# Kernel optimization log

Hardware: AMD Instinct MI355X
Metric: run time of the kernel (lower is better)

The kernel has to match this reference:

```python
import jax, jax.numpy as jnp
import numpy as np

CUTOFFS = [0, 19997, 39997, 199997, 267735]  # cutoff_ends
SIZES = [19997, 20000, 160000, 67738]
DEMBS = [1024, 256, 64, 16]  # d_embed // div_val**i, div_val=4
N, D_PROJ = 1024, 1024


def setup_inputs() -> dict:
    key = jax.random.key(0)
    ks = jax.random.split(key, 20)
    inp = {
        "hidden": jax.random.normal(ks[0], (N, D_PROJ), jnp.float32),
        "target": jax.random.randint(ks[1], (N,), 0, CUTOFFS[-1], dtype=jnp.int64),
    }
    for i in range(4):
        inp[f"W{i}"] = 0.02 * jax.random.normal(ks[2 + 3 * i], (SIZES[i], DEMBS[i]), jnp.float32)
        inp[f"b{i}"] = jnp.zeros((SIZES[i],), jnp.float32)
        inp[f"p{i}"] = 0.02 * jax.random.normal(ks[3 + 3 * i], (D_PROJ, DEMBS[i]), jnp.float32)
    inp["cluster_weight"] = 0.02 * jax.random.normal(ks[14], (3, DEMBS[0]), jnp.float32)
    inp["cluster_bias"] = jnp.zeros((3,), jnp.float32)
    return inp


def _logit(hidden, W, b, p):
    # einsum('bd,de,ev->bv', hidden, proj, weight.T) + bias
    return (hidden @ p) @ W.T + b


def reference(hidden, target, W0, b0, p0, W1, b1, p1, W2, b2, p2, W3, b3, p3,
              cluster_weight, cluster_bias):
    n = hidden.shape[0]
    rows = jnp.arange(n)
    shortlist = W0.shape[0]  # 19997

    # head cluster: shortlist vocab + 3 cluster logits
    head_w = jnp.concatenate([W0, cluster_weight], axis=0)   # [shortlist+3, d_embed]
    head_b = jnp.concatenate([b0, cluster_bias], axis=0)
    head_lp = jax.nn.log_softmax(_logit(hidden, head_w, head_b, p0), axis=-1)  # [N, shortlist+3]

    masks = [target < CUTOFFS[1]]
    lps = [head_lp[rows, jnp.clip(target, 0, shortlist - 1)]]

    for i, (W, b, p) in enumerate([(W1, b1, p1), (W2, b2, p2), (W3, b3, p3)], start=1):
        l_idx, r_idx = CUTOFFS[i], CUTOFFS[i + 1]
        tail_lp = jax.nn.log_softmax(_logit(hidden, W, b, p), axis=-1)  # [N, r-l]
        rel = jnp.clip(target - l_idx, 0, r_idx - l_idx - 1)
        lps.append(head_lp[:, shortlist + i - 1] + tail_lp[rows, rel])
        masks.append((target >= l_idx) & (target < r_idx))

    logprob = jnp.select(masks, lps)
    return -logprob  # nll, shape [N]
```

## Files before the change

### kernel.cpp

```cpp
#include <hip/hip_runtime.h>
#include <stdint.h>

typedef short v8s __attribute__((ext_vector_type(8)));
typedef float f4 __attribute__((ext_vector_type(4)));
typedef unsigned short u16;
typedef unsigned int u32;

#define CUT1 19997
#define CUT2 39997
#define CUT3 199997
#define NROWS 1024
#define LDP 1360

#define NG_HEAD 157
#define NG_T1 40
#define NG_T2 157
#define NG_T3 67

__device__ __forceinline__ u32 pack2(float a, float b) {
    return (__float_as_uint(a) >> 16) | (__float_as_uint(b) & 0xffff0000u);
}
__device__ __forceinline__ float b2f(u16 h) { return __uint_as_float(((u32)h) << 16); }
__device__ __forceinline__ u16 f2b(float f) { return (u16)(__float_as_uint(f) >> 16); }

__device__ __forceinline__ void gload16(const void* g, void* l) {
    __builtin_amdgcn_global_load_lds(
        (const __attribute__((address_space(1))) u32*)g,
        (__attribute__((address_space(3))) u32*)l, 16, 0, 0);
}

__device__ __forceinline__ void cast8(const float* __restrict__ in, u16* __restrict__ out, size_t j) {
    const float4* p = (const float4*)(in + j * 8);
    float4 a = p[0], b = p[1];
    uint4 o = { pack2(a.x, a.y), pack2(a.z, a.w), pack2(b.x, b.y), pack2(b.z, b.w) };
    *(uint4*)(out + j * 8) = o;
}

__global__ __launch_bounds__(256) void prep_small_k(
    const float* __restrict__ hidden,
    const float* __restrict__ p0, const float* __restrict__ p1,
    const float* __restrict__ p2, const float* __restrict__ p3,
    const int* __restrict__ target,
    u16* __restrict__ hb, u16* __restrict__ pTb,
    int* __restrict__ cnt, int* __restrict__ slot,
    int* __restrict__ rowmap)
{
    int bid = blockIdx.x;
    int tid = threadIdx.x;

    if (bid < 512) {
        cast8(hidden, hb, bid * 256 + tid);
        return;
    }
    if (bid < 1888) {
        int b = bid - 512;
        const float* src; int d, rowOff, bx, by;
        if (b < 1024)      { src = p0; d = 1024; rowOff = 0;    bx = b & 31;          by = b >> 5; }
        else if (b < 1280) { src = p1; d = 256;  rowOff = 1024; bx = (b - 1024) & 7;  by = (b - 1024) >> 3; }
        else if (b < 1344) { src = p2; d = 64;   rowOff = 1280; bx = (b - 1280) & 1;  by = (b - 1280) >> 1; }
        else               { src = p3; d = 16;   rowOff = 1344; bx = 0;               by = b - 1344; }
        __shared__ float tile[32][33];
        int tx = tid & 31, ty = tid >> 5;
        int x = bx * 32 + tx;
        int ybase = by * 32;
#pragma unroll
        for (int j = 0; j < 4; ++j) {
            int r = ty + j * 8;
            tile[r][tx] = (x < d) ? src[(size_t)(ybase + r) * d + x] : 0.f;
        }
        __syncthreads();
#pragma unroll
        for (int j = 0; j < 4; ++j) {
            int x2 = bx * 32 + ty + j * 8;
            if (x2 < d) pTb[(size_t)(rowOff + x2) * 1024 + ybase + tx] = f2b(tile[tx][ty + j * 8]);
        }
        return;
    }

    __shared__ int lcnt[3];
    for (int i = tid; i < 3072; i += 256) rowmap[i] = 0;
    if (tid < 3) lcnt[tid] = 0;
    __syncthreads();
    for (int r = tid; r < NROWS; r += 256) {
        int t = target[r];
        int c = (t < CUT1) ? -1 : (t < CUT2) ? 0 : (t < CUT3) ? 1 : 2;
        int s = -1;
        if (c >= 0) {
            s = atomicAdd(&lcnt[c], 1);
            rowmap[c * 1024 + s] = r;
        }
        slot[r] = s;
    }
    __syncthreads();
    if (tid < 3) cnt[tid] = lcnt[tid];
}

template<int MODE, int NCOL, int K>
__device__ __forceinline__ void gemm_body(
    u16* __restrict__ As, u16* __restrict__ Bs, float* __restrict__ bsm,
    const u16* __restrict__ A, int lda, const int* __restrict__ rowmap,
    const u16* __restrict__ B, int ldb,
    const float* __restrict__ bias, int N,
    u16* __restrict__ Cout, int ldc,
    float* __restrict__ pout, const int* __restrict__ count,
    int bx, int byg)
{
    constexpr int nk = K / 32;
    constexpr int total = NCOL * nk;

    const int tid = threadIdx.x;
    const int rbase = bx * 128;
    if (MODE == 1 && count) {
        int c = *count;
        if (rbase >= ((c + 127) & ~127)) return;
    }
    const int wave = tid >> 6, lane = tid & 63;
    const int l4 = lane & 15, quad = lane >> 4;
    const int wg = (wave >> 1) * 4;
    const int cg = (wave & 1) * 4;
    const int wr = wg * 16, wc = cg * 16;

    const int g0 = tid >> 6, seg0 = (tid >> 4) & 3, r0 = tid & 15;
    const int s1i = 256 + tid;
    const int g1 = s1i >> 6, seg1 = (s1i >> 4) & 3, r1 = s1i & 15;

    const u16 *Asrc0, *Asrc1;
    {
        int ar0 = rbase + g0 * 16 + r0, ar1 = rbase + g1 * 16 + r1;
        if (rowmap) { ar0 = rowmap[ar0]; ar1 = rowmap[ar1]; }
        Asrc0 = A + (size_t)ar0 * lda + seg0 * 8;
        Asrc1 = A + (size_t)ar1 * lda + seg1 * 8;
    }

    if (MODE == 1) {
        const int cb0 = byg * (NCOL * 128);
        for (int i2 = tid; i2 < NCOL * 128; i2 += 256) {
            int col = cb0 + i2;
            bsm[i2] = (col < N) ? bias[col] : 0.f;
        }
        __syncthreads();
    }

    auto stage = [&](int s2) {
        const int buf = s2 % 3;
        const int kk = (s2 % nk) * 32;
        const int ct = s2 / nk;
        const int cb = (byg * NCOL + ct) * 128;
        int bc0 = cb + g0 * 16 + r0; if (bc0 >= N) bc0 = N - 1;
        int bc1 = cb + g1 * 16 + r1; if (bc1 >= N) bc1 = N - 1;
        u16* bA = As + buf * 4096;
        u16* bB = Bs + buf * 4096;
        gload16(Asrc0 + kk, bA + tid * 8);
        gload16(Asrc1 + kk, bA + (256 + tid) * 8);
        gload16(B + (size_t)bc0 * ldb + seg0 * 8 + kk, bB + tid * 8);
        gload16(B + (size_t)bc1 * ldb + seg1 * 8 + kk, bB + (256 + tid) * 8);
    };

    float part[4][4];
    if (MODE == 1) {
#pragma unroll
        for (int r = 0; r < 4; ++r)
#pragma unroll
            for (int g = 0; g < 4; ++g) part[r][g] = 0.f;
    }

    stage(0);
    if (total > 1) stage(1);

    const f4 zero4 = {0.f, 0.f, 0.f, 0.f};
    f4 acc[4][4];

#pragma unroll
    for (int s = 0; s < total; ++s) {
        if (s + 1 < total) asm volatile("s_waitcnt vmcnt(4)" ::: "memory");
        else               asm volatile("s_waitcnt vmcnt(0)" ::: "memory");
        __builtin_amdgcn_sched_barrier(0);
        __builtin_amdgcn_s_barrier();
        __builtin_amdgcn_sched_barrier(0);

        const int buf = s % 3;
        const u16* Ab = As + buf * 4096;
        const u16* Bb = Bs + buf * 4096;
        v8s af[4], bf[4];
#pragma unroll
        for (int r = 0; r < 4; ++r)
            af[r] = *(const v8s*)&Ab[((wg + r) * 64 + quad * 16 + l4) * 8];
#pragma unroll
        for (int c = 0; c < 4; ++c)
            bf[c] = *(const v8s*)&Bb[((cg + c) * 64 + quad * 16 + l4) * 8];

        if (s + 2 < total) stage(s + 2);

        if ((s % nk) == 0) {
#pragma unroll
            for (int r = 0; r < 4; ++r)
#pragma unroll
                for (int c = 0; c < 4; ++c) acc[r][c] = zero4;
        }

        __builtin_amdgcn_s_setprio(1);
#pragma unroll
        for (int r = 0; r < 4; ++r)
#pragma unroll
            for (int c = 0; c < 4; ++c)
                acc[r][c] = __builtin_amdgcn_mfma_f32_16x16x32_bf16(af[r], bf[c], acc[r][c], 0, 0, 0);
        __builtin_amdgcn_s_setprio(0);

        if ((s % nk) == nk - 1) {
            const int ct = s / nk;
            const int cbase = (byg * NCOL + ct) * 128;
            if (MODE == 0) {
#pragma unroll
                for (int c = 0; c < 4; ++c) {
                    int col = cbase + wc + c * 16 + l4;
                    if (col < N) {
#pragma unroll
                        for (int r = 0; r < 4; ++r)
#pragma unroll
                            for (int g = 0; g < 4; ++g) {
                                int row = rbase + wr + r * 16 + quad * 4 + g;
                                Cout[(size_t)row * ldc + col] = f2b(acc[r][c][g]);
                            }
                    }
                }
            } else {
#pragma unroll
                for (int c = 0; c < 4; ++c) {
                    int col = cbase + wc + c * 16 + l4;
                    if (col < N) {
                        float bb = bsm[ct * 128 + wc + c * 16 + l4];
#pragma unroll
                        for (int r = 0; r < 4; ++r)
#pragma unroll
                            for (int g = 0; g < 4; ++g)
                                part[r][g] += __expf(acc[r][c][g] + bb);
                    }
                }
            }
        }
    }

    if (MODE == 1) {
#pragma unroll
        for (int off = 1; off < 16; off <<= 1)
#pragma unroll
            for (int r = 0; r < 4; ++r)
#pragma unroll
                for (int g = 0; g < 4; ++g)
                    part[r][g] += __shfl_xor(part[r][g], off);
        float v = part[0][0];
#pragma unroll
        for (int r = 0; r < 4; ++r)
#pragma unroll
            for (int g = 0; g < 4; ++g)
                if (l4 == r * 4 + g) v = part[r][g];
        int rowoff = (l4 >> 2) * 16 + quad * 4 + (l4 & 3);
        float* lbuf = (float*)As;
        __syncthreads();
        lbuf[(wave & 1) * 128 + wr + rowoff] = v;
        __syncthreads();
        if (tid < 128) pout[rbase + tid] = lbuf[tid] + lbuf[128 + tid];
    }
}

#define CP_E0 2559616
#define CP_E1 3199616
#define CP_E2 4479616
__global__ __launch_bounds__(256, 3) void castproj_k(
    const u16* __restrict__ hb, const u16* __restrict__ pTb, u16* __restrict__ proj,
    const float* __restrict__ W0, const float* __restrict__ W1,
    const float* __restrict__ W2, const float* __restrict__ W3,
    u16* __restrict__ W0b, u16* __restrict__ W1b,
    u16* __restrict__ W2b, u16* __restrict__ W3b)
{
    __shared__ __align__(16) u16 As[3 * 4096];
    __shared__ __align__(16) u16 Bs[3 * 4096];
    int bid = blockIdx.x;
    if (bid < 128) {
        int x = bid & 7, j = bid >> 3;
        int byg = x * 2 + (j >> 3), bx = j & 7;
        if (byg >= 11) return;
        gemm_body<0, 1, 1024>(As, Bs, nullptr, hb, 1024, nullptr, pTb, 1024, nullptr, 1360,
                              proj, LDP, nullptr, nullptr, bx, byg);
        return;
    }
    int i = (bid - 128) * 256 + threadIdx.x;
    if (i < CP_E0) { cast8(W0, W0b, i); return; }
    if (i < CP_E1) { cast8(W1, W1b, i - CP_E0); return; }
    if (i < CP_E2) { cast8(W2, W2b, i - CP_E1); return; }
    int r = i - CP_E2;
    if (r >= 67738) return;
    const float4* p = (const float4*)(W3 + (size_t)r * 16);
    float4 a = p[0], b = p[1], c = p[2], d = p[3];
    uint4 o0 = { pack2(a.x, a.y), pack2(a.z, a.w), pack2(b.x, b.y), pack2(b.z, b.w) };
    uint4 o1 = { pack2(c.x, c.y), pack2(c.z, c.w), pack2(d.x, d.y), pack2(d.z, d.w) };
    uint4 z = { 0, 0, 0, 0 };
    uint4* q = (uint4*)(W3b + (size_t)r * 32);
    q[0] = o0; q[1] = o1; q[2] = z; q[3] = z;
}

#define SE_GRID 3456
__global__ __launch_bounds__(256, 3) void sumexp_k(
    const u16* __restrict__ proj,
    const u16* __restrict__ W0b, const u16* __restrict__ W1b,
    const u16* __restrict__ W2b, const u16* __restrict__ W3b,
    const float* __restrict__ b0, const float* __restrict__ b1,
    const float* __restrict__ b2, const float* __restrict__ b3,
    float* __restrict__ Ph, float* __restrict__ Pt1,
    float* __restrict__ Pt2, float* __restrict__ Pt3,
    const int* __restrict__ rmap, const int* __restrict__ cnt)
{
    __shared__ __align__(16) u16 As[3 * 4096];
    __shared__ __align__(16) u16 Bs[3 * 4096];
    __shared__ __align__(16) float bsm[1024];
    int bid = blockIdx.x;
    if (bid < 1280) {
        int x = bid & 7, j = bid >> 3;
        int byg = x * 20 + (j >> 3), bx = j & 7;
        if (byg >= NG_HEAD) return;
        gemm_body<1, 1, 1024>(As, Bs, bsm, proj, LDP, nullptr, W0b, 1024, b0, CUT1,
                              nullptr, 0, Ph + (size_t)byg * 1024, nullptr, bx, byg);
    } else if (bid < 1600) {
        int rel = bid - 1280;
        int x = rel & 7, j = rel >> 3;
        int byg = x * 5 + (j >> 3), bx = j & 7;
        gemm_body<1, 4, 256>(As, Bs, bsm, proj + 1024, LDP, rmap, W1b, 256, b1, 20000,
                             nullptr, 0, Pt1 + (size_t)byg * 1024, cnt + 0, bx, byg);
    } else if (bid < 2880) {
        int rel = bid - 1600;
        int x = rel & 7, j = rel >> 3;
        int byg = x * 20 + (j >> 3), bx = j & 7;
        if (byg >= NG_T2) return;
        gemm_body<1, 8, 64>(As, Bs, bsm, proj + 1280, LDP, rmap + 1024, W2b, 64, b2, 160000,
                            nullptr, 0, Pt2 + (size_t)byg * 1024, cnt + 1, bx, byg);
    } else {
        int rel = bid - 2880;
        int x = rel & 7, j = rel >> 3;
        int byg = x * 9 + (j >> 3), bx = j & 7;
        if (byg >= NG_T3) return;
        gemm_body<1, 8, 32>(As, Bs, bsm, proj + 1344, LDP, rmap + 2048, W3b, 32, b3, 67738,
                            nullptr, 0, Pt3 + (size_t)byg * 1024, cnt + 2, bx, byg);
    }
}

__global__ __launch_bounds__(256) void final_k(
    const u16* __restrict__ proj, const int* __restrict__ target, const int* __restrict__ slot,
    const float* __restrict__ cw, const float* __restrict__ cb,
    const float* __restrict__ W0, const float* __restrict__ b0,
    const float* __restrict__ W1, const float* __restrict__ b1,
    const float* __restrict__ W2, const float* __restrict__ b2,
    const float* __restrict__ W3, const float* __restrict__ b3,
    const float* __restrict__ Ph, const float* __restrict__ Pt1,
    const float* __restrict__ Pt2, const float* __restrict__ Pt3,
    float* __restrict__ out)
{
    int row = blockIdx.x * 4 + (threadIdx.x >> 6);
    int lane = threadIdx.x & 63;
    const u16* pr = proj + (size_t)row * LDP;

    float c0 = 0.f, c1 = 0.f, c2 = 0.f;
    for (int k = lane; k < 1024; k += 64) {
        float pv = b2f(pr[k]);
        c0 += pv * cw[k]; c1 += pv * cw[1024 + k]; c2 += pv * cw[2048 + k];
    }
    float hs = 0.f;
    for (int g = lane; g < NG_HEAD; g += 64) hs += Ph[g * 1024 + row];

    int t = target[row];
    const float* W; const float* bb; int K, off, rel;
    const float* Pc = Ph; int gc = 0;
    if (t < CUT1)      { W = W0; bb = b0; K = 1024; off = 0;    rel = t; }
    else if (t < CUT2) { W = W1; bb = b1; K = 256;  off = 1024; rel = t - CUT1; Pc = Pt1; gc = NG_T1; }
    else if (t < CUT3) { W = W2; bb = b2; K = 64;   off = 1280; rel = t - CUT2; Pc = Pt2; gc = NG_T2; }
    else               { W = W3; bb = b3; K = 16;   off = 1344; rel = t - CUT3; Pc = Pt3; gc = NG_T3; }

    float ts = 0.f;
    int s = slot[row];
    if (s >= 0) {
        for (int g = lane; g < gc; g += 64) ts += Pc[g * 1024 + s];
    }
    float acc = 0.f;
    const float* wr = W + (size_t)rel * K;
    for (int k = lane; k < K; k += 64) acc += b2f(pr[off + k]) * wr[k];

#pragma unroll
    for (int o2 = 1; o2 < 64; o2 <<= 1) {
        c0 += __shfl_xor(c0, o2); c1 += __shfl_xor(c1, o2); c2 += __shfl_xor(c2, o2);
        hs += __shfl_xor(hs, o2); ts += __shfl_xor(ts, o2); acc += __shfl_xor(acc, o2);
    }

    if (lane == 0) {
        c0 += cb[0]; c1 += cb[1]; c2 += cb[2];
        float tl = acc + bb[rel];
        float lseh = __logf(hs + __expf(c0) + __expf(c1) + __expf(c2));
        float lp;
        if (t < CUT1) lp = tl - lseh;
        else {
            int c = (t < CUT2) ? 0 : (t < CUT3) ? 1 : 2;
            float cc = (c == 0) ? c0 : (c == 1) ? c1 : c2;
            lp = (cc - lseh) + (tl - __logf(ts));
        }
        out[row] = -lp;
    }
}

__global__ void cast_bf16_k(const float* __restrict__ in, u16* __restrict__ out, int n8) {
    int i = blockIdx.x * 256 + threadIdx.x;
    if (i >= n8) return;
    cast8(in, out, i);
}

__global__ void transpose_f_k(const float* __restrict__ in, float* __restrict__ out, int d, int rowOff) {
    __shared__ float tile[32][33];
    int tx = threadIdx.x, ty = threadIdx.y;
    int x = blockIdx.x * 32 + tx;
    int ybase = blockIdx.y * 32;
#pragma unroll
    for (int j = 0; j < 4; ++j) {
        int r = ty + j * 8;
        tile[r][tx] = (x < d) ? in[(size_t)(ybase + r) * d + x] : 0.f;
    }
    __syncthreads();
#pragma unroll
    for (int j = 0; j < 4; ++j) {
        int x2 = blockIdx.x * 32 + ty + j * 8;
        if (x2 < d) out[(size_t)(rowOff + x2) * 1024 + ybase + tx] = tile[tx][ty + j * 8];
    }
}

__global__ __launch_bounds__(256) void gemm_tn_k(
    const u16* __restrict__ A, int lda,
    const float* __restrict__ B, int ldb,
    const float* __restrict__ bias, int N, int K,
    u16* __restrict__ Cout, int ldc, float* __restrict__ rowsum)
{
    int tid = threadIdx.x;
    int wave = tid >> 6, lane = tid & 63;
    int l4 = lane & 15, quad = lane >> 4;
    int rbase = blockIdx.x * 16;
    int cbase = blockIdx.y * 256 + wave * 64;

    f4 acc[4] = {};
    v8s zero8 = {0, 0, 0, 0, 0, 0, 0, 0};
    const u16* arow = A + (size_t)(rbase + l4) * lda;
    int nk = (K + 31) >> 5;
    for (int kt = 0; kt < nk; ++kt) {
        int kk = (kt << 5) + quad * 8;
        v8s a = (kk < K) ? *(const v8s*)(arow + kk) : zero8;
#pragma unroll
        for (int t = 0; t < 4; ++t) {
            int col = cbase + t * 16 + l4;
            v8s b = zero8;
            if ((col < N) && (kk < K)) {
                const float* bp = B + (size_t)col * ldb + kk;
                float4 f0 = *(const float4*)bp;
                float4 f1 = *(const float4*)(bp + 4);
                union { uint4 u; v8s s; } bu;
                bu.u.x = pack2(f0.x, f0.y); bu.u.y = pack2(f0.z, f0.w);
                bu.u.z = pack2(f1.x, f1.y); bu.u.w = pack2(f1.z, f1.w);
                b = bu.s;
            }
            acc[t] = __builtin_amdgcn_mfma_f32_16x16x32_bf16(a, b, acc[t], 0, 0, 0);
        }
    }
    if (Cout) {
#pragma unroll
        for (int t = 0; t < 4; ++t) {
            int col = cbase + t * 16 + l4;
            if (col < N) {
#pragma unroll
                for (int r = 0; r < 4; ++r)
                    Cout[(size_t)(rbase + quad * 4 + r) * ldc + col] = f2b(acc[t][r]);
            }
        }
    } else {
        float part[4] = {0.f, 0.f, 0.f, 0.f};
#pragma unroll
        for (int t = 0; t < 4; ++t) {
            int col = cbase + t * 16 + l4;
            if (col < N) {
                float bb = bias[col];
#pragma unroll
                for (int r = 0; r < 4; ++r) part[r] += __expf(acc[t][r] + bb);
            }
        }
#pragma unroll
        for (int off = 1; off < 16; off <<= 1)
#pragma unroll
            for (int r = 0; r < 4; ++r) part[r] += __shfl_xor(part[r], off);
        if (l4 < 4) {
            float v = (l4 == 0) ? part[0] : (l4 == 1) ? part[1] : (l4 == 2) ? part[2] : part[3];
            atomicAdd(&rowsum[rbase + quad * 4 + l4], v);
        }
    }
}

__global__ __launch_bounds__(256) void gather_k(
    const u16* __restrict__ proj, const int* __restrict__ target,
    const float* __restrict__ cw, const float* __restrict__ cb,
    const float* __restrict__ W0, const float* __restrict__ b0,
    const float* __restrict__ W1, const float* __restrict__ b1,
    const float* __restrict__ W2, const float* __restrict__ b2,
    const float* __restrict__ W3, const float* __restrict__ b3,
    float* __restrict__ rs_head, float* __restrict__ cl, float* __restrict__ tl)
{
    int row = blockIdx.x * 4 + (threadIdx.x >> 6);
    int lane = threadIdx.x & 63;
    const u16* pr = proj + (size_t)row * LDP;

    float c0 = 0.f, c1 = 0.f, c2 = 0.f;
    for (int k = lane; k < 1024; k += 64) {
        float pv = b2f(pr[k]);
        c0 += pv * cw[k]; c1 += pv * cw[1024 + k]; c2 += pv * cw[2048 + k];
    }
#pragma unroll
    for (int off = 1; off < 64; off <<= 1) {
        c0 += __shfl_xor(c0, off); c1 += __shfl_xor(c1, off); c2 += __shfl_xor(c2, off);
    }
    int t = target[row];
    const float* W; const float* bb; int K, off, rel;
    if (t < CUT1)      { W = W0; bb = b0; K = 1024; off = 0;    rel = t; }
    else if (t < CUT2) { W = W1; bb = b1; K = 256;  off = 1024; rel = t - CUT1; }
    else if (t < CUT3) { W = W2; bb = b2; K = 64;   off = 1280; rel = t - CUT2; }
    else               { W = W3; bb = b3; K = 16;   off = 1344; rel = t - CUT3; }
    float acc = 0.f;
    const float* wr = W + (size_t)rel * K;
    for (int k = lane; k < K; k += 64) acc += b2f(pr[off + k]) * wr[k];
#pragma unroll
    for (int o2 = 1; o2 < 64; o2 <<= 1) acc += __shfl_xor(acc, o2);
    if (lane == 0) {
        c0 += cb[0]; c1 += cb[1]; c2 += cb[2];
        cl[row * 3 + 0] = c0; cl[row * 3 + 1] = c1; cl[row * 3 + 2] = c2;
        atomicAdd(&rs_head[row], __expf(c0) + __expf(c1) + __expf(c2));
        tl[row] = acc + bb[rel];
    }
}

__global__ void finalize_full_k(const int* __restrict__ target, const float* __restrict__ rs,
                                const float* __restrict__ cl, const float* __restrict__ tl,
                                float* __restrict__ out)
{
    int i = blockIdx.x * 256 + threadIdx.x;
    if (i >= NROWS) return;
    int t = target[i];
    float lseh = __logf(rs[i]);
    float lp;
    if (t < CUT1) lp = tl[i] - lseh;
    else {
        int c = (t < CUT2) ? 0 : (t < CUT3) ? 1 : 2;
        lp = (cl[i * 3 + c] - lseh) + (tl[i] - __logf(rs[(c + 1) * 1024 + i]));
    }
    out[i] = -lp;
}

extern "C" void kernel_launch(void* const* d_in, const int* in_sizes, int n_in,
                              void* d_out, int out_size, void* d_ws, size_t ws_size,
                              hipStream_t stream)
{
    const float* hidden = (const float*)d_in[0];
    const int*   target = (const int*)d_in[1];
    const float* W0 = (const float*)d_in[2];
    const float* b0 = (const float*)d_in[3];
    const float* p0 = (const float*)d_in[4];
    const float* W1 = (const float*)d_in[5];
    const float* b1 = (const float*)d_in[6];
    const float* p1 = (const float*)d_in[7];
    const float* W2 = (const float*)d_in[8];
    const float* b2 = (const float*)d_in[9];
    const float* p2 = (const float*)d_in[10];
    const float* W3 = (const float*)d_in[11];
    const float* b3 = (const float*)d_in[12];
    const float* p3 = (const float*)d_in[13];
    const float* cw = (const float*)d_in[14];
    const float* cb = (const float*)d_in[15];
    float* out = (float*)d_out;
    char* w = (char*)d_ws;

    if (ws_size >= 84000000ull) {
        u16*   hb   = (u16*)(w + 0);
        u16*   pTb  = (u16*)(w + 2097152);
        float* Ph   = (float*)(w + 0);
        float* Pt1  = (float*)(w + 643072);
        float* Pt2  = (float*)(w + 806912);
        float* Pt3  = (float*)(w + 1449984);
        u16*   proj = (u16*)(w + 4882432);
        u16*   W0b  = (u16*)(w + 7667712);
        u16*   W1b  = (u16*)(w + 48621568);
        u16*   W2b  = (u16*)(w + 58861568);
        u16*   W3b  = (u16*)(w + 79341568);
        int*   cnt  = (int*)(w + 83693184);
        int*   slot = (int*)(w + 83693200);
        int*   rmap = (int*)(w + 83697296);

        prep_small_k<<<1889, 256, 0, stream>>>(hidden, p0, p1, p2, p3, target,
                                               hb, pTb, cnt, slot, rmap);

        castproj_k<<<17892, 256, 0, stream>>>(hb, pTb, proj,
                                              W0, W1, W2, W3, W0b, W1b, W2b, W3b);

        sumexp_k<<<SE_GRID, 256, 0, stream>>>(proj, W0b, W1b, W2b, W3b,
                                              b0, b1, b2, b3,
                                              Ph, Pt1, Pt2, Pt3, rmap, cnt);

        final_k<<<256, 256, 0, stream>>>(proj, target, slot, cw, cb,
                                         W0, b0, W1, b1, W2, b2, W3, b3,
                                         Ph, Pt1, Pt2, Pt3, out);
    } else {
        float* pT   = (float*)w;
        u16*   hb   = (u16*)(w + 5570560);
        u16*   proj = (u16*)(w + 7667712);
        float* rs   = (float*)(w + 10452992);
        float* cl   = (float*)(w + 10469376);
        float* tl   = (float*)(w + 10481664);
        dim3 tb(32, 8);

        hipMemsetAsync(rs, 0, 4 * 1024 * sizeof(float), stream);
        cast_bf16_k<<<512, 256, 0, stream>>>(hidden, hb, 131072);
        transpose_f_k<<<dim3(32, 32), tb, 0, stream>>>(p0, pT, 1024, 0);
        transpose_f_k<<<dim3(8, 32),  tb, 0, stream>>>(p1, pT, 256, 1024);
        transpose_f_k<<<dim3(2, 32),  tb, 0, stream>>>(p2, pT, 64, 1280);
        transpose_f_k<<<dim3(1, 32),  tb, 0, stream>>>(p3, pT, 16, 1344);

        gemm_tn_k<<<dim3(64, 6), 256, 0, stream>>>(hb, 1024, pT, 1024, nullptr,
                                                   1360, 1024, proj, LDP, nullptr);
        gemm_tn_k<<<dim3(64, 79), 256, 0, stream>>>(proj, LDP, W0, 1024, b0,
                                                    CUT1, 1024, nullptr, 0, rs);
        gemm_tn_k<<<dim3(64, 79), 256, 0, stream>>>(proj + 1024, LDP, W1, 256, b1,
                                                    20000, 256, nullptr, 0, rs + 1024);
        gemm_tn_k<<<dim3(64, 625), 256, 0, stream>>>(proj + 1280, LDP, W2, 64, b2,
                                                     160000, 64, nullptr, 0, rs + 2048);
        gemm_tn_k<<<dim3(64, 265), 256, 0, stream>>>(proj + 1344, LDP, W3, 16, b3,
                                                     67738, 16, nullptr, 0, rs + 3072);

        gather_k<<<256, 256, 0, stream>>>(proj, target, cw, cb,
                                          W0, b0, W1, b1, W2, b2, W3, b3, rs, cl, tl);
        finalize_full_k<<<4, 256, 0, stream>>>(target, rs, cl, tl, out);
    }
}
```

Baseline: 356.8 us.

## Load fp32 vocab weights directly in sumexp GEMM, drop separate bf16 cast pass

Removes the pre-cast of W0, W1 and W2 to bf16 in a separate pass. The sumexp GEMM now streams the fp32 weights into shared memory via global_load_lds and packs them to bf16 in registers before the MFMA. This saves one write and one re-read of roughly 40MB of bf16 copies. In exchange, each GEMM stage moves twice the B bytes and the B shared buffer doubles, so occupancy drops from 3 to 2 blocks per CU. The W3 cast moves into the prep kernel and the projection GEMM becomes its own kernel.

```diff
diff --git a/kernel.cpp b/kernel.cpp
--- a/kernel.cpp
+++ b/kernel.cpp
@@ -40,8 +40,8 @@
     const float* __restrict__ hidden,
     const float* __restrict__ p0, const float* __restrict__ p1,
     const float* __restrict__ p2, const float* __restrict__ p3,
-    const int* __restrict__ target,
-    u16* __restrict__ hb, u16* __restrict__ pTb,
+    const int* __restrict__ target, const float* __restrict__ W3,
+    u16* __restrict__ hb, u16* __restrict__ pTb, u16* __restrict__ W3b,
     int* __restrict__ cnt, int* __restrict__ slot,
     int* __restrict__ rowmap)
 {
@@ -76,30 +76,42 @@
         }
         return;
     }
-
-    __shared__ int lcnt[3];
-    for (int i = tid; i < 3072; i += 256) rowmap[i] = 0;
-    if (tid < 3) lcnt[tid] = 0;
-    __syncthreads();
-    for (int r = tid; r < NROWS; r += 256) {
-        int t = target[r];
-        int c = (t < CUT1) ? -1 : (t < CUT2) ? 0 : (t < CUT3) ? 1 : 2;
-        int s = -1;
-        if (c >= 0) {
-            s = atomicAdd(&lcnt[c], 1);
-            rowmap[c * 1024 + s] = r;
-        }
-        slot[r] = s;
-    }
-    __syncthreads();
-    if (tid < 3) cnt[tid] = lcnt[tid];
-}
-
-template<int MODE, int NCOL, int K>
+    if (bid == 1888) {
+        __shared__ int lcnt[3];
+        for (int i = tid; i < 3072; i += 256) rowmap[i] = 0;
+        if (tid < 3) lcnt[tid] = 0;
+        __syncthreads();
+        for (int r = tid; r < NROWS; r += 256) {
+            int t = target[r];
+            int c = (t < CUT1) ? -1 : (t < CUT2) ? 0 : (t < CUT3) ? 1 : 2;
+            int s = -1;
+            if (c >= 0) {
+                s = atomicAdd(&lcnt[c], 1);
+                rowmap[c * 1024 + s] = r;
+            }
+            slot[r] = s;
+        }
+        __syncthreads();
+        if (tid < 3) cnt[tid] = lcnt[tid];
+        return;
+    }
+    int r = (bid - 1889) * 256 + tid;
+    if (r >= 67738) return;
+    const float4* p = (const float4*)(W3 + (size_t)r * 16);
+    float4 a = p[0], b = p[1], c = p[2], d = p[3];
+    uint4 o0 = { pack2(a.x, a.y), pack2(a.z, a.w), pack2(b.x, b.y), pack2(b.z, b.w) };
+    uint4 o1 = { pack2(c.x, c.y), pack2(c.z, c.w), pack2(d.x, d.y), pack2(d.z, d.w) };
+    uint4 z = { 0, 0, 0, 0 };
+    uint4* q = (uint4*)(W3b + (size_t)r * 32);
+    q[0] = o0; q[1] = o1; q[2] = z; q[3] = z;
+}
+#define PREP_GRID (1889 + 265)
+
+template<int MODE, int NCOL, int K, int BF32>
 __device__ __forceinline__ void gemm_body(
     u16* __restrict__ As, u16* __restrict__ Bs, float* __restrict__ bsm,
     const u16* __restrict__ A, int lda, const int* __restrict__ rowmap,
-    const u16* __restrict__ B, int ldb,
+    const void* __restrict__ Bv, int ldb,
     const float* __restrict__ bias, int N,
     u16* __restrict__ Cout, int ldc,
     float* __restrict__ pout, const int* __restrict__ count,
@@ -107,6 +119,7 @@
 {
     constexpr int nk = K / 32;
     constexpr int total = NCOL * nk;
+    constexpr int BSTRIDE = BF32 ? 8192 : 4096;
 
     const int tid = threadIdx.x;
     const int rbase = bx * 128;
@@ -123,6 +136,9 @@
     const int g0 = tid >> 6, seg0 = (tid >> 4) & 3, r0 = tid & 15;
     const int s1i = 256 + tid;
     const int g1 = s1i >> 6, seg1 = (s1i >> 4) & 3, r1 = s1i & 15;
+
+    const u16* Bh = (const u16*)Bv;
+    const float* Bf = (const float*)Bv;
 
     const u16 *Asrc0, *Asrc1;
     {
@@ -149,11 +165,20 @@
         int bc0 = cb + g0 * 16 + r0; if (bc0 >= N) bc0 = N - 1;
         int bc1 = cb + g1 * 16 + r1; if (bc1 >= N) bc1 = N - 1;
         u16* bA = As + buf * 4096;
-        u16* bB = Bs + buf * 4096;
+        u16* bB = Bs + buf * BSTRIDE;
         gload16(Asrc0 + kk, bA + tid * 8);
         gload16(Asrc1 + kk, bA + (256 + tid) * 8);
-        gload16(B + (size_t)bc0 * ldb + seg0 * 8 + kk, bB + tid * 8);
-        gload16(B + (size_t)bc1 * ldb + seg1 * 8 + kk, bB + (256 + tid) * 8);
+        if constexpr (BF32) {
+            const float* q0 = Bf + (size_t)bc0 * ldb + seg0 * 8 + kk;
+            const float* q1 = Bf + (size_t)bc1 * ldb + seg1 * 8 + kk;
+            gload16(q0,     bB + tid * 8);
+            gload16(q0 + 4, bB + 4096 + tid * 8);
+            gload16(q1,     bB + (256 + tid) * 8);
+            gload16(q1 + 4, bB + 4096 + (256 + tid) * 8);
+        } else {
+            gload16(Bh + (size_t)bc0 * ldb + seg0 * 8 + kk, bB + tid * 8);
+            gload16(Bh + (size_t)bc1 * ldb + seg1 * 8 + kk, bB + (256 + tid) * 8);
+        }
     };
 
     float part[4][4];
@@ -172,22 +197,39 @@
 
 #pragma unroll
     for (int s = 0; s < total; ++s) {
-        if (s + 1 < total) asm volatile("s_waitcnt vmcnt(4)" ::: "memory");
-        else               asm volatile("s_waitcnt vmcnt(0)" ::: "memory");
+        if (s + 1 < total) {
+            if constexpr (BF32) asm volatile("s_waitcnt vmcnt(6)" ::: "memory");
+            else                asm volatile("s_waitcnt vmcnt(4)" ::: "memory");
+        } else {
+            asm volatile("s_waitcnt vmcnt(0)" ::: "memory");
+        }
         __builtin_amdgcn_sched_barrier(0);
         __builtin_amdgcn_s_barrier();
         __builtin_amdgcn_sched_barrier(0);
 
         const int buf = s % 3;
         const u16* Ab = As + buf * 4096;
-        const u16* Bb = Bs + buf * 4096;
+        const u16* Bb = Bs + buf * BSTRIDE;
         v8s af[4], bf[4];
 #pragma unroll
         for (int r = 0; r < 4; ++r)
             af[r] = *(const v8s*)&Ab[((wg + r) * 64 + quad * 16 + l4) * 8];
-#pragma unroll
-        for (int c = 0; c < 4; ++c)
-            bf[c] = *(const v8s*)&Bb[((cg + c) * 64 + quad * 16 + l4) * 8];
+        if constexpr (BF32) {
+#pragma unroll
+            for (int c = 0; c < 4; ++c) {
+                int slt = (cg + c) * 64 + quad * 16 + l4;
+                float4 f0 = *(const float4*)&Bb[slt * 8];
+                float4 f1 = *(const float4*)&Bb[4096 + slt * 8];
+                union { uint4 u; v8s s; } bu;
+                bu.u.x = pack2(f0.x, f0.y); bu.u.y = pack2(f0.z, f0.w);
+                bu.u.z = pack2(f1.x, f1.y); bu.u.w = pack2(f1.z, f1.w);
+                bf[c] = bu.s;
+            }
+        } else {
+#pragma unroll
+            for (int c = 0; c < 4; ++c)
+                bf[c] = *(const v8s*)&Bb[((cg + c) * 64 + quad * 16 + l4) * 8];
+        }
 
         if (s + 2 < total) stage(s + 2);
 
@@ -263,47 +305,24 @@
     }
 }
 
-#define CP_E0 2559616
-#define CP_E1 3199616
-#define CP_E2 4479616
-__global__ __launch_bounds__(256, 3) void castproj_k(
-    const u16* __restrict__ hb, const u16* __restrict__ pTb, u16* __restrict__ proj,
-    const float* __restrict__ W0, const float* __restrict__ W1,
-    const float* __restrict__ W2, const float* __restrict__ W3,
-    u16* __restrict__ W0b, u16* __restrict__ W1b,
-    u16* __restrict__ W2b, u16* __restrict__ W3b)
+__global__ __launch_bounds__(256, 3) void projgemm_k(
+    const u16* __restrict__ hb, const u16* __restrict__ pTb, u16* __restrict__ proj)
 {
     __shared__ __align__(16) u16 As[3 * 4096];
     __shared__ __align__(16) u16 Bs[3 * 4096];
     int bid = blockIdx.x;
-    if (bid < 128) {
-        int x = bid & 7, j = bid >> 3;
-        int byg = x * 2 + (j >> 3), bx = j & 7;
-        if (byg >= 11) return;
-        gemm_body<0, 1, 1024>(As, Bs, nullptr, hb, 1024, nullptr, pTb, 1024, nullptr, 1360,
-                              proj, LDP, nullptr, nullptr, bx, byg);
-        return;
-    }
-    int i = (bid - 128) * 256 + threadIdx.x;
-    if (i < CP_E0) { cast8(W0, W0b, i); return; }
-    if (i < CP_E1) { cast8(W1, W1b, i - CP_E0); return; }
-    if (i < CP_E2) { cast8(W2, W2b, i - CP_E1); return; }
-    int r = i - CP_E2;
-    if (r >= 67738) return;
-    const float4* p = (const float4*)(W3 + (size_t)r * 16);
-    float4 a = p[0], b = p[1], c = p[2], d = p[3];
-    uint4 o0 = { pack2(a.x, a.y), pack2(a.z, a.w), pack2(b.x, b.y), pack2(b.z, b.w) };
-    uint4 o1 = { pack2(c.x, c.y), pack2(c.z, c.w), pack2(d.x, d.y), pack2(d.z, d.w) };
-    uint4 z = { 0, 0, 0, 0 };
-    uint4* q = (uint4*)(W3b + (size_t)r * 32);
-    q[0] = o0; q[1] = o1; q[2] = z; q[3] = z;
+    int x = bid & 7, j = bid >> 3;
+    int byg = x * 2 + (j >> 3), bx = j & 7;
+    if (byg >= 11) return;
+    gemm_body<0, 1, 1024, 0>(As, Bs, nullptr, hb, 1024, nullptr, pTb, 1024, nullptr, 1360,
+                             proj, LDP, nullptr, nullptr, bx, byg);
 }
 
 #define SE_GRID 3456
-__global__ __launch_bounds__(256, 3) void sumexp_k(
+__global__ __launch_bounds__(256, 2) void sumexp_k(
     const u16* __restrict__ proj,
-    const u16* __restrict__ W0b, const u16* __restrict__ W1b,
-    const u16* __restrict__ W2b, const u16* __restrict__ W3b,
+    const float* __restrict__ W0, const float* __restrict__ W1,
+    const float* __restrict__ W2, const u16* __restrict__ W3b,
     const float* __restrict__ b0, const float* __restrict__ b1,
     const float* __restrict__ b2, const float* __restrict__ b3,
     float* __restrict__ Ph, float* __restrict__ Pt1,
@@ -311,35 +330,35 @@
     const int* __restrict__ rmap, const int* __restrict__ cnt)
 {
     __shared__ __align__(16) u16 As[3 * 4096];
-    __shared__ __align__(16) u16 Bs[3 * 4096];
+    __shared__ __align__(16) u16 Bs[3 * 8192];
     __shared__ __align__(16) float bsm[1024];
     int bid = blockIdx.x;
     if (bid < 1280) {
         int x = bid & 7, j = bid >> 3;
         int byg = x * 20 + (j >> 3), bx = j & 7;
         if (byg >= NG_HEAD) return;
-        gemm_body<1, 1, 1024>(As, Bs, bsm, proj, LDP, nullptr, W0b, 1024, b0, CUT1,
-                              nullptr, 0, Ph + (size_t)byg * 1024, nullptr, bx, byg);
+        gemm_body<1, 1, 1024, 1>(As, Bs, bsm, proj, LDP, nullptr, W0, 1024, b0, CUT1,
+                                 nullptr, 0, Ph + (size_t)byg * 1024, nullptr, bx, byg);
     } else if (bid < 1600) {
         int rel = bid - 1280;
         int x = rel & 7, j = rel >> 3;
         int byg = x * 5 + (j >> 3), bx = j & 7;
-        gemm_body<1, 4, 256>(As, Bs, bsm, proj + 1024, LDP, rmap, W1b, 256, b1, 20000,
-                             nullptr, 0, Pt1 + (size_t)byg * 1024, cnt + 0, bx, byg);
+        gemm_body<1, 4, 256, 1>(As, Bs, bsm, proj + 1024, LDP, rmap, W1, 256, b1, 20000,
+                                nullptr, 0, Pt1 + (size_t)byg * 1024, cnt + 0, bx, byg);
     } else if (bid < 2880) {
         int rel = bid - 1600;
         int x = rel & 7, j = rel >> 3;
         int byg = x * 20 + (j >> 3), bx = j & 7;
         if (byg >= NG_T2) return;
-        gemm_body<1, 8, 64>(As, Bs, bsm, proj + 1280, LDP, rmap + 1024, W2b, 64, b2, 160000,
-                            nullptr, 0, Pt2 + (size_t)byg * 1024, cnt + 1, bx, byg);
+        gemm_body<1, 8, 64, 1>(As, Bs, bsm, proj + 1280, LDP, rmap + 1024, W2, 64, b2, 160000,
+                               nullptr, 0, Pt2 + (size_t)byg * 1024, cnt + 1, bx, byg);
     } else {
         int rel = bid - 2880;
         int x = rel & 7, j = rel >> 3;
         int byg = x * 9 + (j >> 3), bx = j & 7;
         if (byg >= NG_T3) return;
-        gemm_body<1, 8, 32>(As, Bs, bsm, proj + 1344, LDP, rmap + 2048, W3b, 32, b3, 67738,
-                            nullptr, 0, Pt3 + (size_t)byg * 1024, cnt + 2, bx, byg);
+        gemm_body<1, 8, 32, 0>(As, Bs, bsm, proj + 1344, LDP, rmap + 2048, W3b, 32, b3, 67738,
+                               nullptr, 0, Pt3 + (size_t)byg * 1024, cnt + 2, bx, byg);
     }
 }
 
@@ -584,21 +603,17 @@
         float* Pt2  = (float*)(w + 806912);
         float* Pt3  = (float*)(w + 1449984);
         u16*   proj = (u16*)(w + 4882432);
-        u16*   W0b  = (u16*)(w + 7667712);
-        u16*   W1b  = (u16*)(w + 48621568);
-        u16*   W2b  = (u16*)(w + 58861568);
         u16*   W3b  = (u16*)(w + 79341568);
         int*   cnt  = (int*)(w + 83693184);
         int*   slot = (int*)(w + 83693200);
         int*   rmap = (int*)(w + 83697296);
 
-        prep_small_k<<<1889, 256, 0, stream>>>(hidden, p0, p1, p2, p3, target,
-                                               hb, pTb, cnt, slot, rmap);
-
-        castproj_k<<<17892, 256, 0, stream>>>(hb, pTb, proj,
-                                              W0, W1, W2, W3, W0b, W1b, W2b, W3b);
-
-        sumexp_k<<<SE_GRID, 256, 0, stream>>>(proj, W0b, W1b, W2b, W3b,
+        prep_small_k<<<PREP_GRID, 256, 0, stream>>>(hidden, p0, p1, p2, p3, target, W3,
+                                                    hb, pTb, W3b, cnt, slot, rmap);
+
+        projgemm_k<<<128, 256, 0, stream>>>(hb, pTb, proj);
+
+        sumexp_k<<<SE_GRID, 256, 0, stream>>>(proj, W0, W1, W2, W3b,
                                               b0, b1, b2, b3,
                                               Ph, Pt1, Pt2, Pt3, rmap, cnt);
 
```

After: 414.5 us. +16.2%, slower.

## Switch GEMM to double-buffered LDS with nested loops for higher occupancy

Applied to the files above, without the earlier changes.

Replaces the fully unrolled triple-buffered pipeline with a nested column/k loop that uses two LDS buffers and a plain __syncthreads per step. The shared bias staging buffer is dropped, and bias is read straight from global memory in the epilogue. Launch bounds are raised from three to four blocks per CU to exploit the smaller LDS footprint. The aim is more occupancy and less code size, at the cost of a shallower prefetch depth (one stage ahead instead of two) and extra global bias loads.

```diff
diff --git a/kernel.cpp b/kernel.cpp
--- a/kernel.cpp
+++ b/kernel.cpp
@@ -97,7 +97,7 @@
 
 template<int MODE, int NCOL, int K>
 __device__ __forceinline__ void gemm_body(
-    u16* __restrict__ As, u16* __restrict__ Bs, float* __restrict__ bsm,
+    u16* __restrict__ As, u16* __restrict__ Bs,
     const u16* __restrict__ A, int lda, const int* __restrict__ rowmap,
     const u16* __restrict__ B, int ldb,
     const float* __restrict__ bias, int N,
@@ -132,17 +132,8 @@
         Asrc1 = A + (size_t)ar1 * lda + seg1 * 8;
     }
 
-    if (MODE == 1) {
-        const int cb0 = byg * (NCOL * 128);
-        for (int i2 = tid; i2 < NCOL * 128; i2 += 256) {
-            int col = cb0 + i2;
-            bsm[i2] = (col < N) ? bias[col] : 0.f;
-        }
-        __syncthreads();
-    }
-
     auto stage = [&](int s2) {
-        const int buf = s2 % 3;
+        const int buf = s2 & 1;
         const int kk = (s2 % nk) * 32;
         const int ct = s2 / nk;
         const int cb = (byg * NCOL + ct) * 128;
@@ -165,76 +156,69 @@
     }
 
     stage(0);
-    if (total > 1) stage(1);
 
     const f4 zero4 = {0.f, 0.f, 0.f, 0.f};
     f4 acc[4][4];
 
-#pragma unroll
-    for (int s = 0; s < total; ++s) {
-        if (s + 1 < total) asm volatile("s_waitcnt vmcnt(4)" ::: "memory");
-        else               asm volatile("s_waitcnt vmcnt(0)" ::: "memory");
-        __builtin_amdgcn_sched_barrier(0);
-        __builtin_amdgcn_s_barrier();
-        __builtin_amdgcn_sched_barrier(0);
-
-        const int buf = s % 3;
-        const u16* Ab = As + buf * 4096;
-        const u16* Bb = Bs + buf * 4096;
-        v8s af[4], bf[4];
+    for (int ct = 0; ct < NCOL; ++ct) {
 #pragma unroll
         for (int r = 0; r < 4; ++r)
-            af[r] = *(const v8s*)&Ab[((wg + r) * 64 + quad * 16 + l4) * 8];
-#pragma unroll
-        for (int c = 0; c < 4; ++c)
-            bf[c] = *(const v8s*)&Bb[((cg + c) * 64 + quad * 16 + l4) * 8];
-
-        if (s + 2 < total) stage(s + 2);
-
-        if ((s % nk) == 0) {
+#pragma unroll
+            for (int c = 0; c < 4; ++c) acc[r][c] = zero4;
+
+#pragma unroll 2
+        for (int kt = 0; kt < nk; ++kt) {
+            const int s = ct * nk + kt;
+            __syncthreads();
+
+            const int buf = s & 1;
+            const u16* Ab = As + buf * 4096;
+            const u16* Bb = Bs + buf * 4096;
+            v8s af[4], bf[4];
 #pragma unroll
             for (int r = 0; r < 4; ++r)
-#pragma unroll
-                for (int c = 0; c < 4; ++c) acc[r][c] = zero4;
-        }
-
-        __builtin_amdgcn_s_setprio(1);
-#pragma unroll
-        for (int r = 0; r < 4; ++r)
+                af[r] = *(const v8s*)&Ab[((wg + r) * 64 + quad * 16 + l4) * 8];
 #pragma unroll
             for (int c = 0; c < 4; ++c)
-                acc[r][c] = __builtin_amdgcn_mfma_f32_16x16x32_bf16(af[r], bf[c], acc[r][c], 0, 0, 0);
-        __builtin_amdgcn_s_setprio(0);
-
-        if ((s % nk) == nk - 1) {
-            const int ct = s / nk;
-            const int cbase = (byg * NCOL + ct) * 128;
-            if (MODE == 0) {
-#pragma unroll
-                for (int c = 0; c < 4; ++c) {
-                    int col = cbase + wc + c * 16 + l4;
-                    if (col < N) {
-#pragma unroll
-                        for (int r = 0; r < 4; ++r)
-#pragma unroll
-                            for (int g = 0; g < 4; ++g) {
-                                int row = rbase + wr + r * 16 + quad * 4 + g;
-                                Cout[(size_t)row * ldc + col] = f2b(acc[r][c][g]);
-                            }
-                    }
+                bf[c] = *(const v8s*)&Bb[((cg + c) * 64 + quad * 16 + l4) * 8];
+
+            if (s + 1 < total) stage(s + 1);
+
+            __builtin_amdgcn_s_setprio(1);
+#pragma unroll
+            for (int r = 0; r < 4; ++r)
+#pragma unroll
+                for (int c = 0; c < 4; ++c)
+                    acc[r][c] = __builtin_amdgcn_mfma_f32_16x16x32_bf16(af[r], bf[c], acc[r][c], 0, 0, 0);
+            __builtin_amdgcn_s_setprio(0);
+        }
+
+        const int cbase = (byg * NCOL + ct) * 128;
+        if (MODE == 0) {
+#pragma unroll
+            for (int c = 0; c < 4; ++c) {
+                int col = cbase + wc + c * 16 + l4;
+                if (col < N) {
+#pragma unroll
+                    for (int r = 0; r < 4; ++r)
+#pragma unroll
+                        for (int g = 0; g < 4; ++g) {
+                            int row = rbase + wr + r * 16 + quad * 4 + g;
+                            Cout[(size_t)row * ldc + col] = f2b(acc[r][c][g]);
+                        }
                 }
-            } else {
-#pragma unroll
-                for (int c = 0; c < 4; ++c) {
-                    int col = cbase + wc + c * 16 + l4;
-                    if (col < N) {
-                        float bb = bsm[ct * 128 + wc + c * 16 + l4];
-#pragma unroll
-                        for (int r = 0; r < 4; ++r)
-#pragma unroll
-                            for (int g = 0; g < 4; ++g)
-                                part[r][g] += __expf(acc[r][c][g] + bb);
-                    }
+            }
+        } else {
+#pragma unroll
+            for (int c = 0; c < 4; ++c) {
+                int col = cbase + wc + c * 16 + l4;
+                if (col < N) {
+                    float bb = bias[col];
+#pragma unroll
+                    for (int r = 0; r < 4; ++r)
+#pragma unroll
+                        for (int g = 0; g < 4; ++g)
+                            part[r][g] += __expf(acc[r][c][g] + bb);
                 }
             }
         }
@@ -266,21 +250,22 @@
 #define CP_E0 2559616
 #define CP_E1 3199616
 #define CP_E2 4479616
-__global__ __launch_bounds__(256, 3) void castproj_k(
+#define CP_GRID 17892
+__global__ __launch_bounds__(256, 4) void castproj_k(
     const u16* __restrict__ hb, const u16* __restrict__ pTb, u16* __restrict__ proj,
     const float* __restrict__ W0, const float* __restrict__ W1,
     const float* __restrict__ W2, const float* __restrict__ W3,
     u16* __restrict__ W0b, u16* __restrict__ W1b,
     u16* __restrict__ W2b, u16* __restrict__ W3b)
 {
-    __shared__ __align__(16) u16 As[3 * 4096];
-    __shared__ __align__(16) u16 Bs[3 * 4096];
+    __shared__ __align__(16) u16 As[2 * 4096];
+    __shared__ __align__(16) u16 Bs[2 * 4096];
     int bid = blockIdx.x;
     if (bid < 128) {
         int x = bid & 7, j = bid >> 3;
         int byg = x * 2 + (j >> 3), bx = j & 7;
         if (byg >= 11) return;
-        gemm_body<0, 1, 1024>(As, Bs, nullptr, hb, 1024, nullptr, pTb, 1024, nullptr, 1360,
+        gemm_body<0, 1, 1024>(As, Bs, hb, 1024, nullptr, pTb, 1024, nullptr, 1360,
                               proj, LDP, nullptr, nullptr, bx, byg);
         return;
     }
@@ -300,7 +285,7 @@
 }
 
 #define SE_GRID 3456
-__global__ __launch_bounds__(256, 3) void sumexp_k(
+__global__ __launch_bounds__(256, 4) void sumexp_k(
     const u16* __restrict__ proj,
     const u16* __restrict__ W0b, const u16* __restrict__ W1b,
     const u16* __restrict__ W2b, const u16* __restrict__ W3b,
@@ -310,35 +295,34 @@
     float* __restrict__ Pt2, float* __restrict__ Pt3,
     const int* __restrict__ rmap, const int* __restrict__ cnt)
 {
-    __shared__ __align__(16) u16 As[3 * 4096];
-    __shared__ __align__(16) u16 Bs[3 * 4096];
-    __shared__ __align__(16) float bsm[1024];
+    __shared__ __align__(16) u16 As[2 * 4096];
+    __shared__ __align__(16) u16 Bs[2 * 4096];
     int bid = blockIdx.x;
     if (bid < 1280) {
         int x = bid & 7, j = bid >> 3;
         int byg = x * 20 + (j >> 3), bx = j & 7;
         if (byg >= NG_HEAD) return;
-        gemm_body<1, 1, 1024>(As, Bs, bsm, proj, LDP, nullptr, W0b, 1024, b0, CUT1,
+        gemm_body<1, 1, 1024>(As, Bs, proj, LDP, nullptr, W0b, 1024, b0, CUT1,
                               nullptr, 0, Ph + (size_t)byg * 1024, nullptr, bx, byg);
     } else if (bid < 1600) {
         int rel = bid - 1280;
         int x = rel & 7, j = rel >> 3;
         int byg = x * 5 + (j >> 3), bx = j & 7;
-        gemm_body<1, 4, 256>(As, Bs, bsm, proj + 1024, LDP, rmap, W1b, 256, b1, 20000,
+        gemm_body<1, 4, 256>(As, Bs, proj + 1024, LDP, rmap, W1b, 256, b1, 20000,
                              nullptr, 0, Pt1 + (size_t)byg * 1024, cnt + 0, bx, byg);
     } else if (bid < 2880) {
         int rel = bid - 1600;
         int x = rel & 7, j = rel >> 3;
         int byg = x * 20 + (j >> 3), bx = j & 7;
         if (byg >= NG_T2) return;
-        gemm_body<1, 8, 64>(As, Bs, bsm, proj + 1280, LDP, rmap + 1024, W2b, 64, b2, 160000,
+        gemm_body<1, 8, 64>(As, Bs, proj + 1280, LDP, rmap + 1024, W2b, 64, b2, 160000,
                             nullptr, 0, Pt2 + (size_t)byg * 1024, cnt + 1, bx, byg);
     } else {
         int rel = bid - 2880;
         int x = rel & 7, j = rel >> 3;
         int byg = x * 9 + (j >> 3), bx = j & 7;
         if (byg >= NG_T3) return;
-        gemm_body<1, 8, 32>(As, Bs, bsm, proj + 1344, LDP, rmap + 2048, W3b, 32, b3, 67738,
+        gemm_body<1, 8, 32>(As, Bs, proj + 1344, LDP, rmap + 2048, W3b, 32, b3, 67738,
                             nullptr, 0, Pt3 + (size_t)byg * 1024, cnt + 2, bx, byg);
     }
 }
@@ -595,8 +579,8 @@
         prep_small_k<<<1889, 256, 0, stream>>>(hidden, p0, p1, p2, p3, target,
                                                hb, pTb, cnt, slot, rmap);
 
-        castproj_k<<<17892, 256, 0, stream>>>(hb, pTb, proj,
-                                              W0, W1, W2, W3, W0b, W1b, W2b, W3b);
+        castproj_k<<<CP_GRID, 256, 0, stream>>>(hb, pTb, proj,
+                                                W0, W1, W2, W3, W0b, W1b, W2b, W3b);
 
         sumexp_k<<<SE_GRID, 256, 0, stream>>>(proj, W0b, W1b, W2b, W3b,
                                               b0, b1, b2, b3,
```

New measurement: 385.6 us. 8.1% more time.
